# Performance work log

Hardware: AMD Instinct MI355X
Metric: run time of the kernel (lower is better)

The kernel has to match this reference:

```python
import jax, jax.numpy as jnp
import numpy as np

D_MODEL = 1024
D_STATE = 16
EPS = 1e-5


def _layernorm(x, g, b):
    mu = x.mean(-1, keepdims=True)
    xc = x - mu
    var = (xc * xc).mean(-1, keepdims=True)
    return xc * jax.lax.rsqrt(var + EPS) * g + b


def setup_inputs() -> dict:
    key = jax.random.key(0)
    ks = jax.random.split(key, 10)
    B, L, d, n = 8, 1024, D_MODEL, D_STATE
    s = 1.0 / np.sqrt(d)
    return {
        "x": jax.random.normal(ks[0], (B, L, d), jnp.float32),
        "h_prev": jnp.zeros((B, d * n), jnp.float32),
        "ln_g": jnp.ones((d,), jnp.float32),
        "ln_b": jnp.zeros((d,), jnp.float32),
        "W_ig": jax.random.uniform(ks[1], (2 * d, d), jnp.float32, -s, s),
        "W_dt": jax.random.uniform(ks[2], (d, d), jnp.float32, -s, s),
        "b_dt": jax.random.uniform(ks[3], (d,), jnp.float32, -s, s),
        "A_log": jax.random.uniform(ks[4], (d, n), jnp.float32, -3.0, -1.0),
        "W_B": jax.random.uniform(ks[5], (n, d), jnp.float32, -s, s),
        "W_C": jax.random.uniform(ks[6], (n, d), jnp.float32, -s, s),
        "D": jnp.ones((d,), jnp.float32),
        "W_out": jax.random.uniform(ks[7], (d, d), jnp.float32, -s, s),
    }


def reference(x, h_prev, ln_g, ln_b, W_ig, W_dt, b_dt, A_log, W_B, W_C, D, W_out):
    Bsz, L, d = x.shape
    n = A_log.shape[1]
    x_norm = _layernorm(x, ln_g, ln_b)
    x_proj = jnp.einsum('bld,ed->ble', x_norm, W_ig)  # [B,L,2d]
    x_in, z = x_proj[..., :d], x_proj[..., d:]
    dt = jax.nn.softplus(jnp.einsum('bld,ed->ble', x_in, W_dt) + b_dt)  # [B,L,d]
    A = -jnp.exp(A_log)  # [d,n]
    B_t = jnp.einsum('bld,nd->bln', x_in, W_B)  # [B,L,n]
    C_t = jnp.einsum('bld,nd->bln', x_in, W_C)  # [B,L,n]
    h0 = h_prev.reshape(Bsz, d, n)

    def step(h, inp):
        dt_t, xin_t, Bt_t, Ct_t = inp  # [B,d],[B,d],[B,n],[B,n]
        dA = jnp.exp(dt_t[..., None] * A)                      # [B,d,n]
        h = dA * h + (dt_t * xin_t)[..., None] * Bt_t[:, None, :]
        y_t = (h * Ct_t[:, None, :]).sum(-1)                   # [B,d]
        return h, y_t

    xs = (jnp.swapaxes(dt, 0, 1), jnp.swapaxes(x_in, 0, 1),
          jnp.swapaxes(B_t, 0, 1), jnp.swapaxes(C_t, 0, 1))
    h_final, y = jax.lax.scan(step, h0, xs)
    y = jnp.swapaxes(y, 0, 1)  # [B,L,d]
    ssm_out = y * jax.nn.silu(z) + x_in * D
    out = jnp.einsum('bld,ed->ble', ssm_out, W_out)
    return (x + out, h_final.reshape(Bsz, -1))
```

## Files before the change

### kernel.cpp

```cpp
#include <hip/hip_runtime.h>
#include <hip/hip_bf16.h>
#include <math.h>

#define DM 1024
#define NS 16
#define BSZ 8
#define LSEQ 1024
#define MROWS (BSZ*LSEQ)
#define CH 32
#define ROWP 36

typedef __bf16 bf16;
typedef bf16 bf16x8 __attribute__((ext_vector_type(8)));
typedef bf16 bf16x4 __attribute__((ext_vector_type(4)));
typedef float f32x4 __attribute__((ext_vector_type(4)));
typedef unsigned int u32;
typedef unsigned short u16;
typedef u32 u32x4 __attribute__((ext_vector_type(4)));

__device__ __forceinline__ void async16(const void* g, void* l) {
  __builtin_amdgcn_global_load_lds((const __attribute__((address_space(1))) void*)g,
                                   (__attribute__((address_space(3))) void*)l,
                                   16, 0, 0);
}

__device__ __forceinline__ float bflo(u32 u) { return __builtin_bit_cast(float, (u32)(u << 16)); }
__device__ __forceinline__ float bfhi(u32 u) { return __builtin_bit_cast(float, (u32)(u & 0xffff0000u)); }

__global__ __launch_bounds__(256)
void preproc(const float* __restrict__ W_ig, const float* __restrict__ W_dt,
             const float* __restrict__ W_B, const float* __restrict__ W_C,
             const float* __restrict__ W_out,
             bf16* __restrict__ wmega, bf16* __restrict__ wstack,
             bf16* __restrict__ wout, bf16* __restrict__ wigT,
             const float* __restrict__ x, const float* __restrict__ ln_g,
             const float* __restrict__ ln_b, bf16* __restrict__ xnorm) {
  __shared__ float tile[64][65];
  const int blk = blockIdx.x;
  const int t = threadIdx.x;

  if (blk < 4128) {
    int i = blk * 256 + t;
    const float* s; bf16* d; int base;
    if (i < 524288)      { s = W_ig;  d = wmega;                           base = 0; }
    else if (i < 786432) { s = W_dt;  d = wstack;                          base = 524288; }
    else if (i < 790528) { s = W_B;   d = wstack + (size_t)DM * DM;        base = 786432; }
    else if (i < 794624) { s = W_C;   d = wstack + (size_t)(DM + NS) * DM; base = 790528; }
    else                 { s = W_out; d = wout;                            base = 794624; }
    int k = i - base;
    float4 v = ((const float4*)s)[k];
    bf16x4 o;
    o.x = (bf16)v.x; o.y = (bf16)v.y; o.z = (bf16)v.z; o.w = (bf16)v.w;
    *(bf16x4*)(d + 4 * (size_t)k) = o;
  } else if (blk < 4384) {
    int tb = blk - 4128;
    const int bk = (tb & 15) * 64;
    const int bd = (tb >> 4) * 64;
    const int c4 = t & 15;
    const int r0 = t >> 4;
#pragma unroll
    for (int p = 0; p < 4; ++p) {
      int r = r0 + p * 16;
      float4 v = *(const float4*)(W_ig + (size_t)(bd + r) * 1024 + bk + c4 * 4);
      tile[r][c4 * 4 + 0] = v.x;
      tile[r][c4 * 4 + 1] = v.y;
      tile[r][c4 * 4 + 2] = v.z;
      tile[r][c4 * 4 + 3] = v.w;
    }
    __syncthreads();
#pragma unroll
    for (int p = 0; p < 4; ++p) {
      int r = r0 + p * 16;
      bf16x4 o;
      o.x = (bf16)tile[c4 * 4 + 0][r];
      o.y = (bf16)tile[c4 * 4 + 1][r];
      o.z = (bf16)tile[c4 * 4 + 2][r];
      o.w = (bf16)tile[c4 * 4 + 3][r];
      *(bf16x4*)(wigT + (size_t)(bk + r) * 1024 + bd + c4 * 4) = o;
    }
  } else {
    const size_t row = blk - 4384;
    float4 v = ((const float4*)(x + row * DM))[t];
    float s = v.x + v.y + v.z + v.w;
    float s2 = v.x*v.x + v.y*v.y + v.z*v.z + v.w*v.w;
#pragma unroll
    for (int m = 1; m < 64; m <<= 1) { s += __shfl_xor(s, m, 64); s2 += __shfl_xor(s2, m, 64); }
    __shared__ float red[8];
    int wave = t >> 6, lane = t & 63;
    if (lane == 0) { red[wave] = s; red[4 + wave] = s2; }
    __syncthreads();
    s  = red[0] + red[1] + red[2] + red[3];
    s2 = red[4] + red[5] + red[6] + red[7];
    float mu  = s * (1.f / DM);
    float var = s2 * (1.f / DM) - mu * mu;
    float inv = rsqrtf(var + 1e-5f);
    float4 gg = ((const float4*)ln_g)[t];
    float4 bb = ((const float4*)ln_b)[t];
    bf16x4 o;
    o.x = (bf16)((v.x - mu) * inv * gg.x + bb.x);
    o.y = (bf16)((v.y - mu) * inv * gg.y + bb.y);
    o.z = (bf16)((v.z - mu) * inv * gg.z + bb.z);
    o.w = (bf16)((v.w - mu) * inv * gg.w + bb.w);
    *(bf16x4*)(xnorm + row * DM + t * 4) = o;
  }
}

template <int EPI, bool SWZ>
__global__ __launch_bounds__(256)
void gemm_bf16(const bf16* __restrict__ A, const bf16* __restrict__ W, int K,
               float* __restrict__ out_f, bf16* __restrict__ out_b,
               u16* __restrict__ out_u1, u16* __restrict__ out_u2,
               const float* __restrict__ aux,
               float* __restrict__ out_f3, float* __restrict__ out_f4) {
  __shared__ bf16 As[3][128 * 32];
  __shared__ bf16 Bs[3][128 * 32];
  int tx, ty;
  if (SWZ) {
    int g = blockIdx.x;
    int xcd = g & 7, slot = g >> 3;
    tx = slot >> 3;
    ty = xcd * 8 + (slot & 7);
  } else {
    tx = blockIdx.x; ty = blockIdx.y;
  }
  const int tid  = threadIdx.x;
  const int wave = tid >> 6, lane = tid & 63;
  const int lr = lane & 15, quad = lane >> 4;
  const size_t arow = (size_t)ty * 128;
  const size_t brow = (size_t)tx * 128;
  f32x4 acc[4][4] = {};

  const int srl  = lane >> 2;
  const int kg   = lane & 3;
  const int srow = wave * 32 + srl;
  const int skc  = (kg ^ ((srl >> 1) & 3)) * 8;
  const bf16* ag = A + (arow + srow) * (size_t)K + skc;
  const bf16* wg = W + (brow + srow) * (size_t)K + skc;

  const int soff = wave * 32 * 32;
  const int ra   = (((wave >> 1) * 64) + lr) * 32 + ((quad ^ ((lr >> 1) & 3)) * 8);
  const int rb   = (((wave & 1)  * 64) + lr) * 32 + ((quad ^ ((lr >> 1) & 3)) * 8);

  bf16 *aw0 = &As[0][soff], *aw1 = &As[1][soff], *aw2 = &As[2][soff];
  bf16 *bw0 = &Bs[0][soff], *bw1 = &Bs[1][soff], *bw2 = &Bs[2][soff];
  const bf16 *ar0 = &As[0][ra], *ar1 = &As[1][ra], *ar2 = &As[2][ra];
  const bf16 *br0 = &Bs[0][rb], *br1 = &Bs[1][rb], *br2 = &Bs[2][rb];

  auto STAGE = [&](bf16* adst, bf16* bdst, int kk) {
    async16(ag + kk,                       adst);
    async16(ag + (size_t)16 * K + kk,      adst + 16 * 32);
    async16(wg + kk,                       bdst);
    async16(wg + (size_t)16 * K + kk,      bdst + 16 * 32);
  };
  auto COMPUTE = [&](const bf16* ap, const bf16* bp) {
    bf16x8 af[4], bfr[4];
#pragma unroll
    for (int i = 0; i < 4; ++i) af[i] = *(const bf16x8*)(ap + i * 16 * 32);
#pragma unroll
    for (int j = 0; j < 4; ++j) bfr[j] = *(const bf16x8*)(bp + j * 16 * 32);
#pragma unroll
    for (int i = 0; i < 4; ++i)
#pragma unroll
      for (int j = 0; j < 4; ++j)
        acc[i][j] = __builtin_amdgcn_mfma_f32_16x16x32_bf16(af[i], bfr[j], acc[i][j], 0, 0, 0);
  };

  STAGE(aw0, bw0, 0);
  STAGE(aw1, bw1, 32);
  asm volatile("s_waitcnt vmcnt(4)" ::: "memory");
  __builtin_amdgcn_s_barrier();

  for (int k0 = 0; k0 < K; k0 += 32) {
    const bool pf = (k0 + 64 < K);
    if (pf) STAGE(aw2, bw2, k0 + 64);
    COMPUTE(ar0, br0);
    if (pf) asm volatile("s_waitcnt vmcnt(4)" ::: "memory");
    else    asm volatile("s_waitcnt vmcnt(0)" ::: "memory");
    __builtin_amdgcn_s_barrier();
    bf16* t0;
    t0 = aw0; aw0 = aw1; aw1 = aw2; aw2 = t0;
    t0 = bw0; bw0 = bw1; bw1 = bw2; bw2 = t0;
    const bf16* t1;
    t1 = ar0; ar0 = ar1; ar1 = ar2; ar2 = t1;
    t1 = br0; br0 = br1; br1 = br2; br2 = t1;
  }

  const size_t mbase = arow + (wave >> 1) * 64;
  const size_t nbase = brow + (wave & 1) * 64;
  if (EPI == 0) {
    if (nbase < 3 * DM) {
      u16* dst; size_t gbase; bool is_dt = false;
      if (nbase < DM)            { dst = out_u1;       gbase = nbase >> 4; }
      else if (nbase < 2 * DM)   { dst = (u16*)out_b;  gbase = (nbase - DM) >> 4; }
      else                       { dst = out_u2;       gbase = (nbase - 2 * DM) >> 4; is_dt = true; }
      bf16* lds_ep = &As[0][0] + (size_t)wave * 1024;
#pragma unroll
      for (int j = 0; j < 4; ++j) {
#pragma unroll
        for (int i = 0; i < 4; ++i)
#pragma unroll
          for (int r = 0; r < 4; ++r) {
            float v = acc[i][j][r];
            if (is_dt) {
              float tt = v + aux[nbase - 2 * DM + j * 16 + lr];
              v = (tt > 20.f) ? tt : __logf(1.f + __expf(tt));
            }
            lds_ep[(i * 16 + quad * 4 + r) * 16 + lr] = (bf16)v;
          }
        u32x4 v0 = *(u32x4*)&lds_ep[lane * 16];
        u32x4 v1 = *(u32x4*)&lds_ep[lane * 16 + 8];
        size_t off = ((gbase + j) * (size_t)MROWS + mbase + lane) * 16;
        *(u32x4*)&dst[off]     = v0;
        *(u32x4*)&dst[off + 8] = v1;
      }
    } else if (nbase < 3 * DM + 2 * NS) {
#pragma unroll
      for (int i = 0; i < 4; ++i)
#pragma unroll
        for (int r = 0; r < 4; ++r) {
          size_t m = mbase + i * 16 + quad * 4 + r;
          out_f3[m * NS + lr] = acc[i][0][r];
          out_f4[m * NS + lr] = acc[i][1][r];
        }
    }
  } else {
#pragma unroll
    for (int i = 0; i < 4; ++i)
#pragma unroll
      for (int j = 0; j < 4; ++j)
#pragma unroll
        for (int r = 0; r < 4; ++r) {
          size_t m = mbase + i * 16 + quad * 4 + r;
          size_t n = nbase + j * 16 + lr;
          float v = acc[i][j][r];
          if (EPI == 2) {
            out_f[m * DM + n] = v + aux[m * DM + n];
          } else {
            out_b[m * (size_t)DM + n] = (bf16)v;
          }
        }
  }
}

__global__ __launch_bounds__(256)
void scan_kernel(const u16* __restrict__ dt_b, const u16* __restrict__ xi_b,
                 const bf16* __restrict__ z_b,
                 const float* __restrict__ B_t, const float* __restrict__ C_t,
                 const float* __restrict__ A_log, const float* __restrict__ h_prev,
                 const float* __restrict__ Dvec,
                 bf16* __restrict__ ssm_out, float* __restrict__ h_final) {
  const int blk = blockIdx.x;
  const int b = blk >> 6;
  const int g = blk & 63;
  const int d0 = g * 16;
  const int t = threadIdx.x;
  const int n = t & 15, dl = t >> 4;
  const int d = d0 + dl;
  const float Ac2 = -__expf(A_log[d * NS + n]) * 1.44269504f;
  float h = h_prev[(size_t)b * DM * NS + (size_t)d * NS + n];

  __shared__ u32   dxs[2][16][ROWP];
  __shared__ float Bsh[2][16][ROWP];
  __shared__ float Csh[2][16][ROWP];
  __shared__ float ys_p[CH][16][17];

  const size_t base_row = (size_t)b * LSEQ;
  const size_t base16 = ((size_t)g * MROWS + base_row) * 16;
  const int l_a = t >> 4, c_a = t & 15;
  const float Dva = Dvec[d0 + c_a];

  {
    dxs[0][c_a][l_a]      = (u32)dt_b[base16 + t]       | ((u32)xi_b[base16 + t] << 16);
    dxs[0][c_a][l_a + 16] = (u32)dt_b[base16 + 256 + t] | ((u32)xi_b[base16 + 256 + t] << 16);
    size_t gB = base_row * NS;
    Bsh[0][c_a][l_a]      = B_t[gB + t];
    Csh[0][c_a][l_a]      = C_t[gB + t];
    Bsh[0][c_a][l_a + 16] = B_t[gB + t + 256];
    Csh[0][c_a][l_a + 16] = C_t[gB + t + 256];
  }
  float za = (float)z_b[base16 + t];
  float zb = (float)z_b[base16 + 256 + t];
  __syncthreads();

  for (int c = 0; c < LSEQ / CH; ++c) {
    const int cur = c & 1, nxt = cur ^ 1;
    u32 pdxa, pdxb; float pBa, pBb, pCa, pCb, pza, pzb;
    if (c + 1 < LSEQ / CH) {
      size_t off = base16 + (size_t)(c + 1) * (CH * 16);
      pdxa = (u32)dt_b[off + t]       | ((u32)xi_b[off + t] << 16);
      pdxb = (u32)dt_b[off + 256 + t] | ((u32)xi_b[off + 256 + t] << 16);
      pza = (float)z_b[off + t]; pzb = (float)z_b[off + 256 + t];
      size_t gB = (base_row + (size_t)(c + 1) * CH) * NS;
      pBa = B_t[gB + t];       pCa = C_t[gB + t];
      pBb = B_t[gB + t + 256]; pCb = C_t[gB + t + 256];
    }
#pragma unroll
    for (int l4 = 0; l4 < CH; l4 += 4) {
      u32x4 dx4 = *(const u32x4*)&dxs[cur][dl][l4];
      f32x4 b4  = *(const f32x4*)&Bsh[cur][n][l4];
      f32x4 c4  = *(const f32x4*)&Csh[cur][n][l4];
#pragma unroll
      for (int i = 0; i < 4; ++i) {
        float dtv = bflo(dx4[i]), xiv = bfhi(dx4[i]);
        float a = __builtin_amdgcn_exp2f(dtv * Ac2);
        h = fmaf(a, h, (dtv * xiv) * b4[i]);
        ys_p[l4 + i][dl][n] = h * c4[i];
      }
    }
    __syncthreads();
    {
      float s1 = 0.f, s2 = 0.f;
#pragma unroll
      for (int k = 0; k < 16; ++k) {
        s1 += ys_p[l_a][c_a][k];
        s2 += ys_p[l_a + 16][c_a][k];
      }
      float x1 = bfhi(dxs[cur][c_a][l_a]);
      float x2 = bfhi(dxs[cur][c_a][l_a + 16]);
      float g1 = za / (1.f + __expf(-za));
      float g2 = zb / (1.f + __expf(-zb));
      size_t l0 = (size_t)c * CH;
      ssm_out[(base_row + l0 + l_a) * DM + d0 + c_a]      = (bf16)(s1 * g1 + x1 * Dva);
      ssm_out[(base_row + l0 + l_a + 16) * DM + d0 + c_a] = (bf16)(s2 * g2 + x2 * Dva);
    }
    if (c + 1 < LSEQ / CH) {
      dxs[nxt][c_a][l_a]      = pdxa;
      dxs[nxt][c_a][l_a + 16] = pdxb;
      Bsh[nxt][c_a][l_a]      = pBa;
      Csh[nxt][c_a][l_a]      = pCa;
      Bsh[nxt][c_a][l_a + 16] = pBb;
      Csh[nxt][c_a][l_a + 16] = pCb;
      za = pza; zb = pzb;
    }
    __syncthreads();
  }
  h_final[(size_t)b * DM * NS + (size_t)d0 * NS + t] = h;
}

extern "C" void kernel_launch(void* const* d_in, const int* in_sizes, int n_in,
                              void* d_out, int out_size, void* d_ws, size_t ws_size,
                              hipStream_t stream) {
  const float* x      = (const float*)d_in[0];
  const float* h_prev = (const float*)d_in[1];
  const float* ln_g   = (const float*)d_in[2];
  const float* ln_b   = (const float*)d_in[3];
  const float* W_ig   = (const float*)d_in[4];
  const float* W_dt   = (const float*)d_in[5];
  const float* b_dt   = (const float*)d_in[6];
  const float* A_log  = (const float*)d_in[7];
  const float* W_B    = (const float*)d_in[8];
  const float* W_C    = (const float*)d_in[9];
  const float* Dvec   = (const float*)d_in[10];
  const float* W_out  = (const float*)d_in[11];

  char* ws = (char*)d_ws;
  size_t off = 0;
  auto alloc = [&](size_t bytes) -> char* {
    char* p = ws + off;
    off += (bytes + 255) & ~(size_t)255;
    return p;
  };
  bf16*  wmega_b = (bf16*)alloc((size_t)3200 * DM * 2);
  bf16*  wstack_b= (bf16*)alloc((size_t)1152 * DM * 2);
  bf16*  wigT_b  = (bf16*)alloc((size_t)DM * DM * 2);
  bf16*  wout_b  = (bf16*)alloc((size_t)DM * DM * 2);
  bf16*  xnorm_b = (bf16*)alloc((size_t)MROWS * DM * 2);
  u16*   xi_w    = (u16*)alloc((size_t)MROWS * DM * 2);
  u16*   dt_w    = (u16*)alloc((size_t)MROWS * DM * 2);
  bf16*  z_bb    = (bf16*)alloc((size_t)MROWS * DM * 2);
  bf16*  ssm_b   = (bf16*)alloc((size_t)MROWS * DM * 2);
  float* Bt      = (float*)alloc((size_t)MROWS * NS * 4);
  float* Ct      = (float*)alloc((size_t)MROWS * NS * 4);
  (void)ws_size; (void)in_sizes; (void)n_in; (void)out_size;

  float* out_main = (float*)d_out;
  float* out_h    = (float*)d_out + (size_t)MROWS * DM;

  preproc<<<12576, 256, 0, stream>>>(W_ig, W_dt, W_B, W_C, W_out,
                                     wmega_b, wstack_b, wout_b, wigT_b,
                                     x, ln_g, ln_b, xnorm_b);

  gemm_bf16<3, false><<<dim3(8, 9), 256, 0, stream>>>(wstack_b, wigT_b, DM,
      nullptr, wmega_b + (size_t)2048 * DM, nullptr, nullptr, nullptr, nullptr, nullptr);

  gemm_bf16<0, true><<<1600, 256, 0, stream>>>(xnorm_b, wmega_b, DM,
      nullptr, z_bb, xi_w, dt_w, b_dt, Bt, Ct);

  scan_kernel<<<512, 256, 0, stream>>>(dt_w, xi_w, z_bb, Bt, Ct, A_log, h_prev,
                                       Dvec, ssm_b, out_h);

  gemm_bf16<2, true><<<512, 256, 0, stream>>>(ssm_b, wout_b, DM,
      out_main, nullptr, nullptr, nullptr, x, nullptr, nullptr);
}
```

Measured before the change: 312.5 us.

## Deepen GEMM LDS pipeline to four stages and widen scan loads

Measured after the change: 338.5 us. 8.3% more time.

```diff
diff --git a/kernel.cpp b/kernel.cpp
--- a/kernel.cpp
+++ b/kernel.cpp
@@ -9,11 +9,13 @@
 #define MROWS (BSZ*LSEQ)
 #define CH 32
 #define ROWP 36
+#define YSP 18
 
 typedef __bf16 bf16;
 typedef bf16 bf16x8 __attribute__((ext_vector_type(8)));
 typedef bf16 bf16x4 __attribute__((ext_vector_type(4)));
 typedef float f32x4 __attribute__((ext_vector_type(4)));
+typedef float f32x2 __attribute__((ext_vector_type(2)));
 typedef unsigned int u32;
 typedef unsigned short u16;
 typedef u32 u32x4 __attribute__((ext_vector_type(4)));
@@ -112,8 +114,8 @@
                u16* __restrict__ out_u1, u16* __restrict__ out_u2,
                const float* __restrict__ aux,
                float* __restrict__ out_f3, float* __restrict__ out_f4) {
-  __shared__ bf16 As[3][128 * 32];
-  __shared__ bf16 Bs[3][128 * 32];
+  __shared__ bf16 As[4][128 * 32];
+  __shared__ bf16 Bs[4][128 * 32];
   int tx, ty;
   if (SWZ) {
     int g = blockIdx.x;
@@ -141,10 +143,10 @@
   const int ra   = (((wave >> 1) * 64) + lr) * 32 + ((quad ^ ((lr >> 1) & 3)) * 8);
   const int rb   = (((wave & 1)  * 64) + lr) * 32 + ((quad ^ ((lr >> 1) & 3)) * 8);
 
-  bf16 *aw0 = &As[0][soff], *aw1 = &As[1][soff], *aw2 = &As[2][soff];
-  bf16 *bw0 = &Bs[0][soff], *bw1 = &Bs[1][soff], *bw2 = &Bs[2][soff];
-  const bf16 *ar0 = &As[0][ra], *ar1 = &As[1][ra], *ar2 = &As[2][ra];
-  const bf16 *br0 = &Bs[0][rb], *br1 = &Bs[1][rb], *br2 = &Bs[2][rb];
+  bf16 *aw0 = &As[0][soff], *aw1 = &As[1][soff], *aw2 = &As[2][soff], *aw3 = &As[3][soff];
+  bf16 *bw0 = &Bs[0][soff], *bw1 = &Bs[1][soff], *bw2 = &Bs[2][soff], *bw3 = &Bs[3][soff];
+  const bf16 *ar0 = &As[0][ra], *ar1 = &As[1][ra], *ar2 = &As[2][ra], *ar3 = &As[3][ra];
+  const bf16 *br0 = &Bs[0][rb], *br1 = &Bs[1][rb], *br2 = &Bs[2][rb], *br3 = &Bs[3][rb];
 
   auto STAGE = [&](bf16* adst, bf16* bdst, int kk) {
     async16(ag + kk,                       adst);
@@ -167,22 +169,24 @@
 
   STAGE(aw0, bw0, 0);
   STAGE(aw1, bw1, 32);
-  asm volatile("s_waitcnt vmcnt(4)" ::: "memory");
+  STAGE(aw2, bw2, 64);
+  asm volatile("s_waitcnt vmcnt(8)" ::: "memory");
   __builtin_amdgcn_s_barrier();
 
   for (int k0 = 0; k0 < K; k0 += 32) {
-    const bool pf = (k0 + 64 < K);
-    if (pf) STAGE(aw2, bw2, k0 + 64);
+    const bool pf = (k0 + 96 < K);
+    if (pf) STAGE(aw3, bw3, k0 + 96);
     COMPUTE(ar0, br0);
-    if (pf) asm volatile("s_waitcnt vmcnt(4)" ::: "memory");
-    else    asm volatile("s_waitcnt vmcnt(0)" ::: "memory");
+    if (pf)              asm volatile("s_waitcnt vmcnt(8)" ::: "memory");
+    else if (k0 + 64 < K) asm volatile("s_waitcnt vmcnt(4)" ::: "memory");
+    else                 asm volatile("s_waitcnt vmcnt(0)" ::: "memory");
     __builtin_amdgcn_s_barrier();
     bf16* t0;
-    t0 = aw0; aw0 = aw1; aw1 = aw2; aw2 = t0;
-    t0 = bw0; bw0 = bw1; bw1 = bw2; bw2 = t0;
+    t0 = aw0; aw0 = aw1; aw1 = aw2; aw2 = aw3; aw3 = t0;
+    t0 = bw0; bw0 = bw1; bw1 = bw2; bw2 = bw3; bw3 = t0;
     const bf16* t1;
-    t1 = ar0; ar0 = ar1; ar1 = ar2; ar2 = t1;
-    t1 = br0; br0 = br1; br1 = br2; br2 = t1;
+    t1 = ar0; ar0 = ar1; ar1 = ar2; ar2 = ar3; ar3 = t1;
+    t1 = br0; br0 = br1; br1 = br2; br2 = br3; br3 = t1;
   }
 
   const size_t mbase = arow + (wave >> 1) * 64;
@@ -262,21 +266,24 @@
   __shared__ u32   dxs[2][16][ROWP];
   __shared__ float Bsh[2][16][ROWP];
   __shared__ float Csh[2][16][ROWP];
-  __shared__ float ys_p[CH][16][17];
+  __shared__ float ys_p[CH][16][YSP];
 
   const size_t base_row = (size_t)b * LSEQ;
   const size_t base16 = ((size_t)g * MROWS + base_row) * 16;
+  const int pl = t >> 3, pc = (2 * t) & 15;
   const int l_a = t >> 4, c_a = t & 15;
   const float Dva = Dvec[d0 + c_a];
 
   {
-    dxs[0][c_a][l_a]      = (u32)dt_b[base16 + t]       | ((u32)xi_b[base16 + t] << 16);
-    dxs[0][c_a][l_a + 16] = (u32)dt_b[base16 + 256 + t] | ((u32)xi_b[base16 + 256 + t] << 16);
+    u32 D = ((const u32*)(dt_b + base16))[t];
+    u32 X = ((const u32*)(xi_b + base16))[t];
+    dxs[0][pc][pl]     = (D & 0xffffu) | (X << 16);
+    dxs[0][pc + 1][pl] = (D >> 16) | (X & 0xffff0000u);
     size_t gB = base_row * NS;
-    Bsh[0][c_a][l_a]      = B_t[gB + t];
-    Csh[0][c_a][l_a]      = C_t[gB + t];
-    Bsh[0][c_a][l_a + 16] = B_t[gB + t + 256];
-    Csh[0][c_a][l_a + 16] = C_t[gB + t + 256];
+    f32x2 B2 = ((const f32x2*)(B_t + gB))[t];
+    f32x2 C2 = ((const f32x2*)(C_t + gB))[t];
+    Bsh[0][pc][pl] = B2.x;  Bsh[0][pc + 1][pl] = B2.y;
+    Csh[0][pc][pl] = C2.x;  Csh[0][pc + 1][pl] = C2.y;
   }
   float za = (float)z_b[base16 + t];
   float zb = (float)z_b[base16 + 256 + t];
@@ -284,15 +291,15 @@
 
   for (int c = 0; c < LSEQ / CH; ++c) {
     const int cur = c & 1, nxt = cur ^ 1;
-    u32 pdxa, pdxb; float pBa, pBb, pCa, pCb, pza, pzb;
+    u32 pD, pX; f32x2 pB2, pC2; float pza, pzb;
     if (c + 1 < LSEQ / CH) {
       size_t off = base16 + (size_t)(c + 1) * (CH * 16);
-      pdxa = (u32)dt_b[off + t]       | ((u32)xi_b[off + t] << 16);
-      pdxb = (u32)dt_b[off + 256 + t] | ((u32)xi_b[off + 256 + t] << 16);
+      pD = ((const u32*)(dt_b + off))[t];
+      pX = ((const u32*)(xi_b + off))[t];
       pza = (float)z_b[off + t]; pzb = (float)z_b[off + 256 + t];
       size_t gB = (base_row + (size_t)(c + 1) * CH) * NS;
-      pBa = B_t[gB + t];       pCa = C_t[gB + t];
-      pBb = B_t[gB + t + 256]; pCb = C_t[gB + t + 256];
+      pB2 = ((const f32x2*)(B_t + gB))[t];
+      pC2 = ((const f32x2*)(C_t + gB))[t];
     }
 #pragma unroll
     for (int l4 = 0; l4 < CH; l4 += 4) {
@@ -309,11 +316,14 @@
     }
     __syncthreads();
     {
+      const f32x2* r1 = (const f32x2*)&ys_p[l_a][c_a][0];
+      const f32x2* r2 = (const f32x2*)&ys_p[l_a + 16][c_a][0];
       float s1 = 0.f, s2 = 0.f;
 #pragma unroll
-      for (int k = 0; k < 16; ++k) {
-        s1 += ys_p[l_a][c_a][k];
-        s2 += ys_p[l_a + 16][c_a][k];
+      for (int k = 0; k < 8; ++k) {
+        f32x2 v1 = r1[k], v2 = r2[k];
+        s1 += v1.x + v1.y;
+        s2 += v2.x + v2.y;
       }
       float x1 = bfhi(dxs[cur][c_a][l_a]);
       float x2 = bfhi(dxs[cur][c_a][l_a + 16]);
@@ -324,12 +334,10 @@
       ssm_out[(base_row + l0 + l_a + 16) * DM + d0 + c_a] = (bf16)(s2 * g2 + x2 * Dva);
     }
     if (c + 1 < LSEQ / CH) {
-      dxs[nxt][c_a][l_a]      = pdxa;
-      dxs[nxt][c_a][l_a + 16] = pdxb;
-      Bsh[nxt][c_a][l_a]      = pBa;
-      Csh[nxt][c_a][l_a]      = pCa;
-      Bsh[nxt][c_a][l_a + 16] = pBb;
-      Csh[nxt][c_a][l_a + 16] = pCb;
+      dxs[nxt][pc][pl]     = (pD & 0xffffu) | (pX << 16);
+      dxs[nxt][pc + 1][pl] = (pD >> 16) | (pX & 0xffff0000u);
+      Bsh[nxt][pc][pl] = pB2.x;  Bsh[nxt][pc + 1][pl] = pB2.y;
+      Csh[nxt][pc][pl] = pC2.x;  Csh[nxt][pc + 1][pl] = pC2.y;
       za = pza; zb = pzb;
     }
     __syncthreads();
```
